# Kernel optimization log

Hardware: AMD Instinct MI355X
Metric: run time of the kernel (lower is better)

## Reference

```python
import jax, jax.numpy as jnp
import numpy as np

NEW_SEQ_LEN = 150  # hard-coded in the original forward


def _interp_one(x, length):
    """PyTorch F.interpolate(mode='linear', align_corners=False) on x[:length].
    x: [T, D] float, length: scalar int. Returns [NEW_SEQ_LEN, D]."""
    lf = length.astype(jnp.float32)
    scale = lf / NEW_SEQ_LEN
    src = (jnp.arange(NEW_SEQ_LEN, dtype=jnp.float32) + 0.5) * scale - 0.5
    src = jnp.maximum(src, 0.0)
    i0 = jnp.floor(src).astype(jnp.int32)
    i0 = jnp.minimum(i0, length - 1)
    i1 = jnp.minimum(i0 + 1, length - 1)
    w = (src - i0.astype(jnp.float32))[:, None]  # [150, 1]
    return x[i0] * (1.0 - w) + x[i1] * w


_interp_batch = jax.vmap(_interp_one)  # ragged per-sample interpolation, fused over batch


def setup_inputs() -> dict:
    key = jax.random.key(0)
    ks = jax.random.split(key, 8)
    B, T, C_IMU, C_EMG, EMB, CSD = 2048, 512, 48, 16, 64, 256
    x_imu = jax.random.normal(ks[0], (B, T, C_IMU), jnp.float32)
    x_emg = jax.random.normal(ks[1], (B, T, C_EMG), jnp.float32)
    lens = jax.random.randint(ks[2], (B,), 160, T + 1, jnp.int32)  # >= NEW_SEQ_LEN
    w_emb_imu = jax.random.normal(ks[3], (C_IMU, EMB), jnp.float32) / np.sqrt(C_IMU)
    b_emb_imu = jnp.zeros((EMB,), jnp.float32)
    w_emb_emg = jax.random.normal(ks[4], (C_EMG, EMB), jnp.float32) / np.sqrt(C_EMG)
    b_emb_emg = jnp.zeros((EMB,), jnp.float32)
    w_proj = jax.random.normal(ks[5], (NEW_SEQ_LEN * EMB, CSD), jnp.float32) / np.sqrt(NEW_SEQ_LEN * EMB)
    b_proj = jnp.zeros((CSD,), jnp.float32)
    return {"x_imu": x_imu, "x_emg": x_emg, "lens": lens,
            "w_emb_imu": w_emb_imu, "b_emb_imu": b_emb_imu,
            "w_emb_emg": w_emb_emg, "b_emb_emg": b_emb_emg,
            "w_proj": w_proj, "b_proj": b_proj}


def reference(x_imu, x_emg, lens, w_emb_imu, b_emb_imu, w_emb_emg, b_emb_emg, w_proj, b_proj):
    B = x_imu.shape[0]
    # embedding nets (per-timestep linear encoders) -> [B, T, 64]
    seq_imu = jnp.einsum('btc,ce->bte', x_imu, w_emb_imu) + b_emb_imu
    seq_emg = jnp.einsum('btc,ce->bte', x_emg, w_emb_emg) + b_emb_emg
    # ragged linear interpolation of each sample's first lens[i] steps to 150
    seq_imu = _interp_batch(seq_imu, lens)  # [B, 150, 64]
    seq_emg = _interp_batch(seq_emg, lens)
    # flatten and project; NOTE: original code applies linear_proj_imu to BOTH
    out_imu = seq_imu.reshape(B, -1) @ w_proj + b_proj
    out_emg = seq_emg.reshape(B, -1) @ w_proj + b_proj
    return (out_imu, out_emg)
```

## Files before the change

### kernel.cpp

```cpp
#include <hip/hip_runtime.h>

#define NEWL 150
#define EMBD 64
#define NCOL 256
#define CIMU 48
#define CEMG 16

#define KIMU (NEWL * CIMU)
#define KEMG (NEWL * CEMG)
#define KSTI 225
#define KSTE 75
#define NCI 5
#define NCE 3

typedef __bf16 bf16x8_t __attribute__((ext_vector_type(8)));
typedef __bf16 bf16x4_t __attribute__((ext_vector_type(4)));
typedef float f32x4_t __attribute__((ext_vector_type(4)));

__device__ __forceinline__ f32x4_t mfma16(bf16x8_t a, bf16x8_t b, f32x4_t c) {
  return __builtin_amdgcn_mfma_f32_16x16x32_bf16(a, b, c, 0, 0, 0);
}

template <int C, int KST>
__device__ void wcomb_body(const float* __restrict__ wemb,
                           const float* __restrict__ wreg_src,
                           __bf16* __restrict__ wpk, int s, int j) {
  float wreg[EMBD];
#pragma unroll
  for (int e = 0; e < EMBD; ++e) wreg[e] = wreg_src[(size_t)e * NCOL];
  const int cb = j >> 4, lr = j & 15;
#pragma unroll
  for (int q = 0; q < C / 8; ++q) {
    const int kq = (s * C) / 8 + q;
    const int ks = kq >> 2, h = kq & 3;
    bf16x8_t tv;
#pragma unroll
    for (int u = 0; u < 8; ++u) {
      const float* we = wemb + (q * 8 + u) * EMBD;
      float acc = 0.f;
#pragma unroll
      for (int e = 0; e < EMBD; ++e) acc = fmaf(we[e], wreg[e], acc);
      tv[u] = (__bf16)acc;
    }
    *(bf16x8_t*)(wpk + (((size_t)cb * KST + ks) * 64 + h * 16 + lr) * 8) = tv;
  }
}

__global__ __launch_bounds__(256) void wcomb_kernel(
    const float* __restrict__ w_emb_imu, const float* __restrict__ w_emb_emg,
    const float* __restrict__ b_emb_imu, const float* __restrict__ b_emb_emg,
    const float* __restrict__ w_proj,
    __bf16* __restrict__ wpk_imu, __bf16* __restrict__ wpk_emg,
    float* __restrict__ bpart) {
  const int s = blockIdx.x;
  const int m = blockIdx.y;
  const int j = threadIdx.x;
  const float* wp_base = w_proj + (size_t)s * EMBD * NCOL + j;
  const float* be = (m == 0) ? b_emb_imu : b_emb_emg;
  float bacc = 0.f;
#pragma unroll
  for (int e = 0; e < EMBD; ++e) bacc = fmaf(be[e], wp_base[(size_t)e * NCOL], bacc);
  bpart[((size_t)m * NEWL + s) * NCOL + j] = bacc;
  if (m == 0)
    wcomb_body<CIMU, KSTI>(w_emb_imu, wp_base, wpk_imu, s, j);
  else
    wcomb_body<CEMG, KSTE>(w_emb_emg, wp_base, wpk_emg, s, j);
}

__global__ __launch_bounds__(512, 2) void fused_kernel(
    const float* __restrict__ x_imu, const float* __restrict__ x_emg,
    const int* __restrict__ lens,
    const __bf16* __restrict__ wpk_imu, const __bf16* __restrict__ wpk_emg,
    const float* __restrict__ b_proj, const float* __restrict__ bpart,
    float* __restrict__ p_imu, float* __restrict__ p_emg,
    float* __restrict__ bias, int B, int T) {
  const int bid = blockIdx.x;
  const int span = B >> 5;
  const int nblk = (NCE + NCI) * span;
  if (bid == nblk) {
    const int j = threadIdx.x;
    if (j < NCOL) {
#pragma unroll
      for (int m = 0; m < 2; ++m) {
        float acc = b_proj[j];
        for (int s = 0; s < NEWL; ++s)
          acc += bpart[((size_t)m * NEWL + s) * NCOL + j];
        bias[m * NCOL + j] = acc;
      }
    }
    return;
  }

  __shared__ __bf16 lds[2][2][3][512];

  const int tid = threadIdx.x;
  const int wv = tid >> 6, l = tid & 63;

  const int cs = bid / span;
  const int mt = bid - cs * span;
  const bool is_imu = cs >= NCE;
  const int c = is_imu ? cs - NCE : cs;

  int g0, NG;
  if (is_imu) { g0 = 15 * c; NG = 15; }
  else        { g0 = (c == 0) ? 0 : (9 + 8 * (c - 1)); NG = c ? 8 : 9; }
  const int ks0 = 3 * g0;
  const int sb = is_imu ? 2 * g0 : 6 * g0;

  const __bf16* Wp = is_imu ? wpk_imu : wpk_emg;
  const int KST = is_imu ? KSTI : KSTE;
  float* P = is_imu ? (p_imu + (size_t)c * B * NCOL) : (p_emg + (size_t)c * B * NCOL);

  const size_t PS = (size_t)KST * 512;
  const __bf16* bg = Wp + ((size_t)(wv * 2) * KST + ks0) * 512 + l * 8;

  const int q = tid & 3, rowb = (tid >> 2) & 1;
  const int pid = tid >> 3, b4 = pid & 31, sl = pid >> 5;
  const int pid_e = tid >> 1;
  const int ble = pid_e / 6, se = pid_e - ble * 6, rowe = tid & 1;
  const bool act = is_imu || (tid < 384);
  const int b_g = mt * 32 + (is_imu ? b4 : (act ? ble : 0));
  int lenv = 1;
  float scale = 0.f;
  if (act) { lenv = lens[b_g]; scale = (float)lenv * (1.0f / 150.0f); }

  float gr[16];
  float wS;
  bf16x8_t bB[6];
  f32x4_t acc00 = {0.f, 0.f, 0.f, 0.f}, acc01 = acc00, acc10 = acc00, acc11 = acc00;

#define ISSUE_GI(g2) do {                                                       \
    const int s_ = sb + (g2) * 2 + sl;                                          \
    float src_ = fmaxf(((float)s_ + 0.5f) * scale - 0.5f, 0.0f);                \
    int i0_ = min((int)src_, lenv - 1);                                         \
    int i1_ = min(i0_ + 1, lenv - 1);                                           \
    wS = src_ - (float)i0_;                                                     \
    const float* r_ =                                                           \
        x_imu + ((size_t)b_g * T + (rowb ? i1_ : i0_)) * CIMU + q * 4;          \
    _Pragma("unroll")                                                           \
    for (int t = 0; t < 3; ++t) {                                               \
      float4 v_ = *(const float4*)(r_ + t * 16);                                \
      gr[t * 4 + 0] = v_.x; gr[t * 4 + 1] = v_.y;                               \
      gr[t * 4 + 2] = v_.z; gr[t * 4 + 3] = v_.w;                               \
    }                                                                           \
  } while (0)

#define LERP_WI(BUF) do {                                                       \
    const float wg_ = wS, om_ = 1.0f - wg_;                                     \
    _Pragma("unroll")                                                           \
    for (int t = 0; t < 3; ++t) {                                               \
      float p0_ = __shfl_xor(gr[t * 4 + 0], 4);                                 \
      float p1_ = __shfl_xor(gr[t * 4 + 1], 4);                                 \
      float p2_ = __shfl_xor(gr[t * 4 + 2], 4);                                 \
      float p3_ = __shfl_xor(gr[t * 4 + 3], 4);                                 \
      if (rowb == 0) {                                                          \
        bf16x4_t o_;                                                            \
        o_[0] = (__bf16)(gr[t * 4 + 0] * om_ + p0_ * wg_);                      \
        o_[1] = (__bf16)(gr[t * 4 + 1] * om_ + p1_ * wg_);                      \
        o_[2] = (__bf16)(gr[t * 4 + 2] * om_ + p2_ * wg_);                      \
        o_[3] = (__bf16)(gr[t * 4 + 3] * om_ + p3_ * wg_);                      \
        const int kq_ = sl * 6 + t * 2 + (q >> 1);                              \
        *(bf16x4_t*)(&lds[BUF][b4 >> 4][kq_ >> 2]                               \
                         [((kq_ & 3) * 16 + (b4 & 15)) * 8 + (q & 1) * 4]) = o_;\
      }                                                                         \
    }                                                                           \
  } while (0)

#define ISSUE_GE(g2) do { if (act) {                                            \
    const int s_ = sb + (g2) * 6 + se;                                          \
    float src_ = fmaxf(((float)s_ + 0.5f) * scale - 0.5f, 0.0f);                \
    int i0_ = min((int)src_, lenv - 1);                                         \
    int i1_ = min(i0_ + 1, lenv - 1);                                           \
    wS = src_ - (float)i0_;                                                     \
    const float* r_ = x_emg + ((size_t)b_g * T + (rowe ? i1_ : i0_)) * CEMG;    \
    _Pragma("unroll")                                                           \
    for (int t = 0; t < 4; ++t) {                                               \
      float4 v_ = *(const float4*)(r_ + t * 4);                                 \
      gr[t * 4 + 0] = v_.x; gr[t * 4 + 1] = v_.y;                               \
      gr[t * 4 + 2] = v_.z; gr[t * 4 + 3] = v_.w;                               \
    }                                                                           \
  } } while (0)

#define LERP_WE(BUF) do { if (act) {                                            \
    const float wg_ = wS, om_ = 1.0f - wg_;                                     \
    _Pragma("unroll")                                                           \
    for (int t2 = 0; t2 < 2; ++t2) {                                            \
      float pv_[8];                                                             \
      _Pragma("unroll")                                                         \
      for (int u = 0; u < 8; ++u) pv_[u] = __shfl_xor(gr[t2 * 8 + u], 1);       \
      if (rowe == 0) {                                                          \
        bf16x8_t o_;                                                            \
        _Pragma("unroll")                                                       \
        for (int u = 0; u < 8; ++u)                                             \
          o_[u] = (__bf16)(gr[t2 * 8 + u] * om_ + pv_[u] * wg_);                \
        const int kq_ = se * 2 + t2;                                            \
        *(bf16x8_t*)(&lds[BUF][ble >> 4][kq_ >> 2]                              \
                         [((kq_ & 3) * 16 + (ble & 15)) * 8]) = o_;             \
      }                                                                         \
    }                                                                           \
  } } while (0)

#define ISSUE_B(g1) do {                                                        \
    const __bf16* pb_ = bg + (size_t)((g1) * 3) * 512;                          \
    _Pragma("unroll")                                                           \
    for (int ks = 0; ks < 3; ++ks) {                                            \
      bB[ks * 2 + 0] = *(const bf16x8_t*)(pb_ + (size_t)ks * 512);              \
      bB[ks * 2 + 1] = *(const bf16x8_t*)(pb_ + PS + (size_t)ks * 512);         \
    }                                                                           \
  } while (0)

#define COMPUTE(Pp) do {                                                        \
    _Pragma("unroll")                                                           \
    for (int ks = 0; ks < 3; ++ks) {                                            \
      bf16x8_t a0_ = *(const bf16x8_t*)(&lds[Pp][0][ks][l * 8]);                \
      bf16x8_t a1_ = *(const bf16x8_t*)(&lds[Pp][1][ks][l * 8]);                \
      acc00 = mfma16(a0_, bB[ks * 2 + 0], acc00);                               \
      acc01 = mfma16(a0_, bB[ks * 2 + 1], acc01);                               \
      acc10 = mfma16(a1_, bB[ks * 2 + 0], acc10);                               \
      acc11 = mfma16(a1_, bB[ks * 2 + 1], acc11);                               \
    }                                                                           \
  } while (0)

  if (is_imu) { ISSUE_GI(0); LERP_WI(0); }
  else        { ISSUE_GE(0); LERP_WE(0); }
  ISSUE_B(0);
  __syncthreads();

  for (int p = 0; p < NG; ++p) {
    const int more = (p + 1 < NG);
    if (more) { if (is_imu) ISSUE_GI(p + 1); else ISSUE_GE(p + 1); }
    COMPUTE(p & 1);
    if (more) ISSUE_B(p + 1);
    if (more) { if (is_imu) LERP_WI((p + 1) & 1); else LERP_WE((p + 1) & 1); }
    __syncthreads();
  }

  const int lh = l >> 4, lr = l & 15;
  float* Pb = P + (size_t)(mt * 32 + lh * 4) * NCOL + wv * 32 + lr;
#pragma unroll
  for (int jj = 0; jj < 4; ++jj) {
    Pb[(size_t)jj * NCOL] = acc00[jj];
    Pb[(size_t)jj * NCOL + 16] = acc01[jj];
    Pb[(size_t)(16 + jj) * NCOL] = acc10[jj];
    Pb[(size_t)(16 + jj) * NCOL + 16] = acc11[jj];
  }
#undef ISSUE_GI
#undef LERP_WI
#undef ISSUE_GE
#undef LERP_WE
#undef ISSUE_B
#undef COMPUTE
}

__global__ __launch_bounds__(256) void combine_kernel(
    const float* __restrict__ bias, const float* __restrict__ p_imu,
    const float* __restrict__ p_emg, float* __restrict__ out, int B) {
  const int b = blockIdx.x, m = blockIdx.y, j = threadIdx.x;
  const size_t n = (size_t)B * NCOL;
  const size_t o = (size_t)b * NCOL + j;
  if (m == 0) {
    float v = bias[j];
#pragma unroll
    for (int c = 0; c < NCI; ++c) v += p_imu[c * n + o];
    out[o] = v;
  } else {
    float v = bias[NCOL + j];
#pragma unroll
    for (int c = 0; c < NCE; ++c) v += p_emg[c * n + o];
    out[n + o] = v;
  }
}

extern "C" void kernel_launch(void* const* d_in, const int* in_sizes, int n_in,
                              void* d_out, int out_size, void* d_ws, size_t ws_size,
                              hipStream_t stream) {
  const float* x_imu     = (const float*)d_in[0];
  const float* x_emg     = (const float*)d_in[1];
  const int*   lens      = (const int*)d_in[2];
  const float* w_emb_imu = (const float*)d_in[3];
  const float* b_emb_imu = (const float*)d_in[4];
  const float* w_emb_emg = (const float*)d_in[5];
  const float* b_emb_emg = (const float*)d_in[6];
  const float* w_proj    = (const float*)d_in[7];
  const float* b_proj    = (const float*)d_in[8];
  float* out = (float*)d_out;

  const int B = in_sizes[2];
  const int T = in_sizes[0] / (B * CIMU);

  char* ws = (char*)d_ws;
  __bf16* wpk_imu = (__bf16*)ws;  ws += (size_t)NCOL * KIMU * 2;
  __bf16* wpk_emg = (__bf16*)ws;  ws += (size_t)NCOL * KEMG * 2;
  float*  bias    = (float*)ws;   ws += 2 * NCOL * 4;
  float*  bpart   = (float*)ws;   ws += (size_t)2 * NEWL * NCOL * 4;
  float*  p_imu   = (float*)ws;   ws += (size_t)NCI * B * NCOL * 4;
  float*  p_emg   = (float*)ws;   ws += (size_t)NCE * B * NCOL * 4;

  wcomb_kernel<<<dim3(NEWL, 2), 256, 0, stream>>>(
      w_emb_imu, w_emb_emg, b_emb_imu, b_emb_emg, w_proj, wpk_imu, wpk_emg, bpart);
  const int span = B >> 5;
  const int nblk = (NCE + NCI) * span + 1;
  fused_kernel<<<nblk, 512, 0, stream>>>(x_imu, x_emg, lens, wpk_imu, wpk_emg,
                                         b_proj, bpart, p_imu, p_emg, bias, B, T);
  combine_kernel<<<dim3(B, 2), 256, 0, stream>>>(bias, p_imu, p_emg, out, B);
}
```

Measured before the change: 81.16 us.

## Warp-specialize fused kernel into producer/consumer waves with LDS ring and flags

Splits each 512-thread block into four consumer waves doing MFMA on 32x64 tiles and four producer waves that gather and interpolate inputs into a 4-deep LDS ring. Hand-off uses volatile per-slot flags with sleep-spin in place of block-wide __syncthreads, so gather latency overlaps compute. Producer threads now load both interpolation rows themselves instead of exchanging them with shuffles. The weight-combine kernel also merges its IMU and EMG grid halves so each w_proj slice is read once. Spin-wait flags risk stalls and ordering bugs, and fewer waves now issue MFMAs.

New measurement: 93.14 us. +14.8%, slower.

```diff
diff --git a/kernel.cpp b/kernel.cpp
--- a/kernel.cpp
+++ b/kernel.cpp
@@ -22,12 +22,9 @@
 }
 
 template <int C, int KST>
-__device__ void wcomb_body(const float* __restrict__ wemb,
-                           const float* __restrict__ wreg_src,
-                           __bf16* __restrict__ wpk, int s, int j) {
-  float wreg[EMBD];
-#pragma unroll
-  for (int e = 0; e < EMBD; ++e) wreg[e] = wreg_src[(size_t)e * NCOL];
+__device__ __forceinline__ void wcomb_body(const float* __restrict__ wemb,
+                                           const float* wreg,
+                                           __bf16* __restrict__ wpk, int s, int j) {
   const int cb = j >> 4, lr = j & 15;
 #pragma unroll
   for (int q = 0; q < C / 8; ++q) {
@@ -52,19 +49,21 @@
     const float* __restrict__ w_proj,
     __bf16* __restrict__ wpk_imu, __bf16* __restrict__ wpk_emg,
     float* __restrict__ bpart) {
-  const int s = blockIdx.x;
-  const int m = blockIdx.y;
-  const int j = threadIdx.x;
+  const int s = blockIdx.x, j = threadIdx.x;
   const float* wp_base = w_proj + (size_t)s * EMBD * NCOL + j;
-  const float* be = (m == 0) ? b_emb_imu : b_emb_emg;
-  float bacc = 0.f;
-#pragma unroll
-  for (int e = 0; e < EMBD; ++e) bacc = fmaf(be[e], wp_base[(size_t)e * NCOL], bacc);
-  bpart[((size_t)m * NEWL + s) * NCOL + j] = bacc;
-  if (m == 0)
-    wcomb_body<CIMU, KSTI>(w_emb_imu, wp_base, wpk_imu, s, j);
-  else
-    wcomb_body<CEMG, KSTE>(w_emb_emg, wp_base, wpk_emg, s, j);
+  float wreg[EMBD];
+#pragma unroll
+  for (int e = 0; e < EMBD; ++e) wreg[e] = wp_base[(size_t)e * NCOL];
+  float bi = 0.f, be = 0.f;
+#pragma unroll
+  for (int e = 0; e < EMBD; ++e) {
+    bi = fmaf(b_emb_imu[e], wreg[e], bi);
+    be = fmaf(b_emb_emg[e], wreg[e], be);
+  }
+  bpart[(size_t)s * NCOL + j] = bi;
+  bpart[((size_t)NEWL + s) * NCOL + j] = be;
+  wcomb_body<CIMU, KSTI>(w_emb_imu, wreg, wpk_imu, s, j);
+  wcomb_body<CEMG, KSTE>(w_emb_emg, wreg, wpk_emg, s, j);
 }
 
 __global__ __launch_bounds__(512, 2) void fused_kernel(
@@ -91,9 +90,17 @@
     return;
   }
 
-  __shared__ __bf16 lds[2][2][3][512];
+  __shared__ __bf16 ring[4][2][3][512];
+  __shared__ int fprod[4][4];
+  __shared__ int fcons[4][4];
 
   const int tid = threadIdx.x;
+  if (tid < 16) ((int*)fprod)[tid] = -1;
+  else if (tid < 32) ((int*)fcons)[tid - 16] = -1;
+  __syncthreads();
+  volatile int* vfp = (volatile int*)&fprod[0][0];
+  volatile int* vfc = (volatile int*)&fcons[0][0];
+
   const int wv = tid >> 6, l = tid & 63;
 
   const int cs = bid / span;
@@ -111,145 +118,205 @@
   const int KST = is_imu ? KSTI : KSTE;
   float* P = is_imu ? (p_imu + (size_t)c * B * NCOL) : (p_emg + (size_t)c * B * NCOL);
 
-  const size_t PS = (size_t)KST * 512;
-  const __bf16* bg = Wp + ((size_t)(wv * 2) * KST + ks0) * 512 + l * 8;
-
-  const int q = tid & 3, rowb = (tid >> 2) & 1;
-  const int pid = tid >> 3, b4 = pid & 31, sl = pid >> 5;
-  const int pid_e = tid >> 1;
-  const int ble = pid_e / 6, se = pid_e - ble * 6, rowe = tid & 1;
-  const bool act = is_imu || (tid < 384);
-  const int b_g = mt * 32 + (is_imu ? b4 : (act ? ble : 0));
-  int lenv = 1;
-  float scale = 0.f;
-  if (act) { lenv = lens[b_g]; scale = (float)lenv * (1.0f / 150.0f); }
-
-  float gr[16];
-  float wS;
-  bf16x8_t bB[6];
-  f32x4_t acc00 = {0.f, 0.f, 0.f, 0.f}, acc01 = acc00, acc10 = acc00, acc11 = acc00;
-
-#define ISSUE_GI(g2) do {                                                       \
-    const int s_ = sb + (g2) * 2 + sl;                                          \
+  if (wv < 4) {
+    const int cw = wv;
+    const int lh = l >> 4, lr = l & 15;
+    const size_t PS = (size_t)KST * 512;
+    const __bf16* bg = Wp + ((size_t)(cw * 4) * KST + ks0) * 512 + l * 8;
+
+    bf16x8_t bB[12];
+    f32x4_t acc[2][4];
+#pragma unroll
+    for (int rp = 0; rp < 2; ++rp)
+#pragma unroll
+      for (int cp = 0; cp < 4; ++cp) acc[rp][cp] = (f32x4_t){0.f, 0.f, 0.f, 0.f};
+
+    for (int g = 0; g < NG; ++g) {
+      {
+        const __bf16* pb = bg + (size_t)(g * 3) * 512;
+#pragma unroll
+        for (int cp = 0; cp < 4; ++cp)
+#pragma unroll
+          for (int ks = 0; ks < 3; ++ks)
+            bB[cp * 3 + ks] =
+                *(const bf16x8_t*)(pb + (size_t)cp * PS + (size_t)ks * 512);
+      }
+      const int slot = g & 3;
+      int seen = 0;
+#pragma unroll
+      for (int pw = 0; pw < 4; ++pw) {
+        int v = vfp[slot * 4 + pw];
+        while (v < g) { __builtin_amdgcn_s_sleep(1); v = vfp[slot * 4 + pw]; }
+        seen += v;
+      }
+      const int poff = seen - 4 * g;
+      const __bf16* ab = &ring[slot][0][0][0] + poff;
+#pragma unroll
+      for (int ks = 0; ks < 3; ++ks) {
+        const bf16x8_t a0 = *(const bf16x8_t*)(ab + (0 * 3 + ks) * 512 + l * 8);
+        const bf16x8_t a1 = *(const bf16x8_t*)(ab + (1 * 3 + ks) * 512 + l * 8);
+#pragma unroll
+        for (int cp = 0; cp < 4; ++cp) {
+          acc[0][cp] = mfma16(a0, bB[cp * 3 + ks], acc[0][cp]);
+          acc[1][cp] = mfma16(a1, bB[cp * 3 + ks], acc[1][cp]);
+        }
+      }
+      __builtin_amdgcn_s_waitcnt(0xC07F);
+      __builtin_amdgcn_sched_barrier(0);
+      if (l == 0) vfc[slot * 4 + cw] = g;
+    }
+    float* Pb = P + (size_t)(mt * 32 + lh * 4) * NCOL + cw * 64 + lr;
+#pragma unroll
+    for (int rp = 0; rp < 2; ++rp)
+#pragma unroll
+      for (int cp = 0; cp < 4; ++cp)
+#pragma unroll
+        for (int jj = 0; jj < 4; ++jj)
+          Pb[(size_t)(rp * 16 + jj) * NCOL + cp * 16] = acc[rp][cp][jj];
+    return;
+  }
+
+  const int pw = wv - 4;
+  const int ptid = tid - 256;
+
+#define P_WAITC(g_, POFF) int POFF;                                             \
+  {                                                                             \
+    const int slot_ = (g_) & 3;                                                 \
+    int seenc_ = 0;                                                             \
+    _Pragma("unroll")                                                           \
+    for (int cw_ = 0; cw_ < 4; ++cw_) {                                         \
+      int v_ = vfc[slot_ * 4 + cw_];                                            \
+      while (v_ < (g_) - 4) { __builtin_amdgcn_s_sleep(1);                      \
+                              v_ = vfc[slot_ * 4 + cw_]; }                      \
+      seenc_ += v_;                                                             \
+    }                                                                           \
+    POFF = seenc_ - (((g_) >= 4) ? 4 * ((g_) - 4) : -4);                        \
+  }
+
+#define P_FLAG(g_) do {                                                         \
+    __builtin_amdgcn_s_waitcnt(0xC07F);                                         \
+    __builtin_amdgcn_sched_barrier(0);                                          \
+    if (l == 0) vfp[((g_) & 3) * 4 + pw] = (g_);                                \
+  } while (0)
+
+  if (is_imu) {
+    const int q = ptid & 3, pair = ptid >> 2;
+    const int b4 = pair & 31, sl = pair >> 5;
+    const int b_g = mt * 32 + b4;
+    const int lenv = lens[b_g];
+    const float scale = (float)lenv * (1.0f / 150.0f);
+    const float* xg = x_imu + (size_t)b_g * T * CIMU + q * 4;
+    float grA[24], grB[24];
+    float wA, wB;
+
+#define PI_ISSUE(g_, GR, WS) do {                                               \
+    const int s_ = sb + (g_) * 2 + sl;                                          \
     float src_ = fmaxf(((float)s_ + 0.5f) * scale - 0.5f, 0.0f);                \
     int i0_ = min((int)src_, lenv - 1);                                         \
     int i1_ = min(i0_ + 1, lenv - 1);                                           \
-    wS = src_ - (float)i0_;                                                     \
-    const float* r_ =                                                           \
-        x_imu + ((size_t)b_g * T + (rowb ? i1_ : i0_)) * CIMU + q * 4;          \
+    WS = src_ - (float)i0_;                                                     \
+    const float* r0_ = xg + (size_t)i0_ * CIMU;                                 \
+    const float* r1_ = xg + (size_t)i1_ * CIMU;                                 \
     _Pragma("unroll")                                                           \
     for (int t = 0; t < 3; ++t) {                                               \
-      float4 v_ = *(const float4*)(r_ + t * 16);                                \
-      gr[t * 4 + 0] = v_.x; gr[t * 4 + 1] = v_.y;                               \
-      gr[t * 4 + 2] = v_.z; gr[t * 4 + 3] = v_.w;                               \
+      float4 v_ = *(const float4*)(r0_ + t * 16);                               \
+      GR[t * 4 + 0] = v_.x; GR[t * 4 + 1] = v_.y;                               \
+      GR[t * 4 + 2] = v_.z; GR[t * 4 + 3] = v_.w;                               \
+      float4 u_ = *(const float4*)(r1_ + t * 16);                               \
+      GR[12 + t * 4 + 0] = u_.x; GR[12 + t * 4 + 1] = u_.y;                     \
+      GR[12 + t * 4 + 2] = u_.z; GR[12 + t * 4 + 3] = u_.w;                     \
     }                                                                           \
   } while (0)
 
-#define LERP_WI(BUF) do {                                                       \
-    const float wg_ = wS, om_ = 1.0f - wg_;                                     \
+#define PI_WRITE(g_, GR, WS, POFF) do {                                         \
+    __bf16* wb_ = &ring[(g_) & 3][0][0][0] + (POFF);                            \
+    const float wg_ = WS, om_ = 1.0f - wg_;                                     \
     _Pragma("unroll")                                                           \
     for (int t = 0; t < 3; ++t) {                                               \
-      float p0_ = __shfl_xor(gr[t * 4 + 0], 4);                                 \
-      float p1_ = __shfl_xor(gr[t * 4 + 1], 4);                                 \
-      float p2_ = __shfl_xor(gr[t * 4 + 2], 4);                                 \
-      float p3_ = __shfl_xor(gr[t * 4 + 3], 4);                                 \
-      if (rowb == 0) {                                                          \
-        bf16x4_t o_;                                                            \
-        o_[0] = (__bf16)(gr[t * 4 + 0] * om_ + p0_ * wg_);                      \
-        o_[1] = (__bf16)(gr[t * 4 + 1] * om_ + p1_ * wg_);                      \
-        o_[2] = (__bf16)(gr[t * 4 + 2] * om_ + p2_ * wg_);                      \
-        o_[3] = (__bf16)(gr[t * 4 + 3] * om_ + p3_ * wg_);                      \
-        const int kq_ = sl * 6 + t * 2 + (q >> 1);                              \
-        *(bf16x4_t*)(&lds[BUF][b4 >> 4][kq_ >> 2]                               \
-                         [((kq_ & 3) * 16 + (b4 & 15)) * 8 + (q & 1) * 4]) = o_;\
-      }                                                                         \
+      bf16x4_t o_;                                                              \
+      _Pragma("unroll")                                                         \
+      for (int u = 0; u < 4; ++u)                                               \
+        o_[u] = (__bf16)(GR[t * 4 + u] * om_ + GR[12 + t * 4 + u] * wg_);       \
+      const int kq_ = sl * 6 + t * 2 + (q >> 1);                                \
+      *(bf16x4_t*)(wb_ + ((b4 >> 4) * 3 + (kq_ >> 2)) * 512 +                   \
+                   ((kq_ & 3) * 16 + (b4 & 15)) * 8 + (q & 1) * 4) = o_;        \
     }                                                                           \
   } while (0)
 
-#define ISSUE_GE(g2) do { if (act) {                                            \
-    const int s_ = sb + (g2) * 6 + se;                                          \
+    PI_ISSUE(0, grA, wA);
+    for (int gp = 0; gp < 15; gp += 2) {
+      if (gp >= NG) break;
+      if (gp + 1 < NG) PI_ISSUE(gp + 1, grB, wB);
+      { P_WAITC(gp, poc0); PI_WRITE(gp, grA, wA, poc0); }
+      P_FLAG(gp);
+      if (gp + 1 >= NG) break;
+      if (gp + 2 < NG) PI_ISSUE(gp + 2, grA, wA);
+      { P_WAITC(gp + 1, poc1); PI_WRITE(gp + 1, grB, wB, poc1); }
+      P_FLAG(gp + 1);
+    }
+  } else {
+    const bool pact = ptid < 192;
+    const int ble = pact ? (ptid / 6) : 0;
+    const int se = pact ? (ptid - (ptid / 6) * 6) : 0;
+    const int b_g = mt * 32 + ble;
+    int lenv = 1;
+    float scale = 0.f;
+    if (pact) { lenv = lens[b_g]; scale = (float)lenv * (1.0f / 150.0f); }
+    float grA[32], grB[32];
+    float wA, wB;
+
+#define PE_ISSUE(g_, GR, WS) do { if (pact) {                                   \
+    const int s_ = sb + (g_) * 6 + se;                                          \
     float src_ = fmaxf(((float)s_ + 0.5f) * scale - 0.5f, 0.0f);                \
     int i0_ = min((int)src_, lenv - 1);                                         \
     int i1_ = min(i0_ + 1, lenv - 1);                                           \
-    wS = src_ - (float)i0_;                                                     \
-    const float* r_ = x_emg + ((size_t)b_g * T + (rowe ? i1_ : i0_)) * CEMG;    \
+    WS = src_ - (float)i0_;                                                     \
+    const float* p0_ = x_emg + ((size_t)b_g * T + i0_) * CEMG;                  \
+    const float* p1_ = x_emg + ((size_t)b_g * T + i1_) * CEMG;                  \
     _Pragma("unroll")                                                           \
     for (int t = 0; t < 4; ++t) {                                               \
-      float4 v_ = *(const float4*)(r_ + t * 4);                                 \
-      gr[t * 4 + 0] = v_.x; gr[t * 4 + 1] = v_.y;                               \
-      gr[t * 4 + 2] = v_.z; gr[t * 4 + 3] = v_.w;                               \
+      float4 v_ = *(const float4*)(p0_ + t * 4);                                \
+      GR[t * 4 + 0] = v_.x; GR[t * 4 + 1] = v_.y;                               \
+      GR[t * 4 + 2] = v_.z; GR[t * 4 + 3] = v_.w;                               \
+      float4 u_ = *(const float4*)(p1_ + t * 4);                                \
+      GR[16 + t * 4 + 0] = u_.x; GR[16 + t * 4 + 1] = u_.y;                     \
+      GR[16 + t * 4 + 2] = u_.z; GR[16 + t * 4 + 3] = u_.w;                     \
     }                                                                           \
   } } while (0)
 
-#define LERP_WE(BUF) do { if (act) {                                            \
-    const float wg_ = wS, om_ = 1.0f - wg_;                                     \
+#define PE_WRITE(g_, GR, WS, POFF) do { if (pact) {                             \
+    __bf16* wb_ = &ring[(g_) & 3][0][0][0] + (POFF);                            \
+    const float wg_ = WS, om_ = 1.0f - wg_;                                     \
     _Pragma("unroll")                                                           \
     for (int t2 = 0; t2 < 2; ++t2) {                                            \
-      float pv_[8];                                                             \
+      bf16x8_t o_;                                                              \
       _Pragma("unroll")                                                         \
-      for (int u = 0; u < 8; ++u) pv_[u] = __shfl_xor(gr[t2 * 8 + u], 1);       \
-      if (rowe == 0) {                                                          \
-        bf16x8_t o_;                                                            \
-        _Pragma("unroll")                                                       \
-        for (int u = 0; u < 8; ++u)                                             \
-          o_[u] = (__bf16)(gr[t2 * 8 + u] * om_ + pv_[u] * wg_);                \
-        const int kq_ = se * 2 + t2;                                            \
-        *(bf16x8_t*)(&lds[BUF][ble >> 4][kq_ >> 2]                              \
-                         [((kq_ & 3) * 16 + (ble & 15)) * 8]) = o_;             \
-      }                                                                         \
+      for (int u = 0; u < 8; ++u)                                               \
+        o_[u] = (__bf16)(GR[t2 * 8 + u] * om_ + GR[16 + t2 * 8 + u] * wg_);     \
+      const int kq_ = se * 2 + t2;                                              \
+      *(bf16x8_t*)(wb_ + ((ble >> 4) * 3 + (kq_ >> 2)) * 512 +                  \
+                   ((kq_ & 3) * 16 + (ble & 15)) * 8) = o_;                     \
     }                                                                           \
   } } while (0)
 
-#define ISSUE_B(g1) do {                                                        \
-    const __bf16* pb_ = bg + (size_t)((g1) * 3) * 512;                          \
-    _Pragma("unroll")                                                           \
-    for (int ks = 0; ks < 3; ++ks) {                                            \
-      bB[ks * 2 + 0] = *(const bf16x8_t*)(pb_ + (size_t)ks * 512);              \
-      bB[ks * 2 + 1] = *(const bf16x8_t*)(pb_ + PS + (size_t)ks * 512);         \
-    }                                                                           \
-  } while (0)
-
-#define COMPUTE(Pp) do {                                                        \
-    _Pragma("unroll")                                                           \
-    for (int ks = 0; ks < 3; ++ks) {                                            \
-      bf16x8_t a0_ = *(const bf16x8_t*)(&lds[Pp][0][ks][l * 8]);                \
-      bf16x8_t a1_ = *(const bf16x8_t*)(&lds[Pp][1][ks][l * 8]);                \
-      acc00 = mfma16(a0_, bB[ks * 2 + 0], acc00);                               \
-      acc01 = mfma16(a0_, bB[ks * 2 + 1], acc01);                               \
-      acc10 = mfma16(a1_, bB[ks * 2 + 0], acc10);                               \
-      acc11 = mfma16(a1_, bB[ks * 2 + 1], acc11);                               \
-    }                                                                           \
-  } while (0)
-
-  if (is_imu) { ISSUE_GI(0); LERP_WI(0); }
-  else        { ISSUE_GE(0); LERP_WE(0); }
-  ISSUE_B(0);
-  __syncthreads();
-
-  for (int p = 0; p < NG; ++p) {
-    const int more = (p + 1 < NG);
-    if (more) { if (is_imu) ISSUE_GI(p + 1); else ISSUE_GE(p + 1); }
-    COMPUTE(p & 1);
-    if (more) ISSUE_B(p + 1);
-    if (more) { if (is_imu) LERP_WI((p + 1) & 1); else LERP_WE((p + 1) & 1); }
-    __syncthreads();
-  }
-
-  const int lh = l >> 4, lr = l & 15;
-  float* Pb = P + (size_t)(mt * 32 + lh * 4) * NCOL + wv * 32 + lr;
-#pragma unroll
-  for (int jj = 0; jj < 4; ++jj) {
-    Pb[(size_t)jj * NCOL] = acc00[jj];
-    Pb[(size_t)jj * NCOL + 16] = acc01[jj];
-    Pb[(size_t)(16 + jj) * NCOL] = acc10[jj];
-    Pb[(size_t)(16 + jj) * NCOL + 16] = acc11[jj];
-  }
-#undef ISSUE_GI
-#undef LERP_WI
-#undef ISSUE_GE
-#undef LERP_WE
-#undef ISSUE_B
-#undef COMPUTE
+    PE_ISSUE(0, grA, wA);
+    for (int gp = 0; gp < 15; gp += 2) {
+      if (gp >= NG) break;
+      if (gp + 1 < NG) PE_ISSUE(gp + 1, grB, wB);
+      { P_WAITC(gp, poc0); PE_WRITE(gp, grA, wA, poc0); }
+      P_FLAG(gp);
+      if (gp + 1 >= NG) break;
+      if (gp + 2 < NG) PE_ISSUE(gp + 2, grA, wA);
+      { P_WAITC(gp + 1, poc1); PE_WRITE(gp + 1, grB, wB, poc1); }
+      P_FLAG(gp + 1);
+    }
+  }
+#undef P_WAITC
+#undef P_FLAG
+#undef PI_ISSUE
+#undef PI_WRITE
+#undef PE_ISSUE
+#undef PE_WRITE
 }
 
 __global__ __launch_bounds__(256) void combine_kernel(
@@ -296,8 +363,9 @@
   float*  p_imu   = (float*)ws;   ws += (size_t)NCI * B * NCOL * 4;
   float*  p_emg   = (float*)ws;   ws += (size_t)NCE * B * NCOL * 4;
 
-  wcomb_kernel<<<dim3(NEWL, 2), 256, 0, stream>>>(
-      w_emb_imu, w_emb_emg, b_emb_imu, b_emb_emg, w_proj, wpk_imu, wpk_emg, bpart);
+  wcomb_kernel<<<NEWL, 256, 0, stream>>>(w_emb_imu, w_emb_emg, b_emb_imu,
+                                         b_emb_emg, w_proj, wpk_imu, wpk_emg,
+                                         bpart);
   const int span = B >> 5;
   const int nblk = (NCE + NCI) * span + 1;
   fused_kernel<<<nblk, 512, 0, stream>>>(x_imu, x_emg, lens, wpk_imu, wpk_emg,
```
